# Performance work log

Hardware: AMD Instinct MI355X
Metric: run time of the kernel (lower is better)

## Reference

```python
import jax, jax.numpy as jnp
import numpy as np

N_SAMPLES = 131072
WINDOW = 2048
HOP = WINDOW // 2            # 1024
N_COEFFS = WINDOW // 2 + 1   # 1025
N_RES = 64
EXPR = 4
BASE_RES = 0.5
RES_FACTOR = 0.99
N_FRAMES = N_SAMPLES // HOP  # 128


def setup_inputs() -> dict:
    key = jax.random.key(0)
    k1, k2, k3, k4 = jax.random.split(key, 4)
    shape = (N_RES, N_COEFFS, EXPR)
    # mirrors torch init: uniform(0.01, 1) base + small deformation
    amp = jax.random.uniform(k1, shape, minval=0.01, maxval=1.0)
    phase = jax.random.uniform(k2, shape, minval=0.01, maxval=1.0)
    decay = jax.random.uniform(k3, shape, minval=0.01, maxval=1.0)
    phase_dither = jax.random.uniform(k4, shape, minval=0.01, maxval=1.0)
    return dict(amp=amp, phase=phase, decay=decay, phase_dither=phase_dither)


def _flat(x):
    # (n_res, n_coeffs, expr) -> (n_res, expr, n_coeffs) -> (n_res*expr, n_coeffs)
    return jnp.transpose(x, (0, 2, 1)).reshape(-1, N_COEFFS)


def reference(amp, phase, decay, phase_dither):
    amp_f, phase_f = _flat(amp), _flat(phase)
    decay_f, dith_f = _flat(decay), _flat(phase_dither)
    B = amp_f.shape[0]  # n_res * expr

    res_span = 1.0 - BASE_RES
    # per-bin per-frame decay coefficient in (base_resonance, ~0.995)
    coeffs = BASE_RES + jax.nn.sigmoid(decay_f) * res_span * RES_FACTOR  # (B, C)
    start_mags = amp_f ** 2                                             # (B, C)
    start_phase = jnp.tanh(phase_f) * np.pi                             # (B, C)
    dither = jnp.tanh(dith_f)                                           # (B, C)

    # frame-wise exponential decay scan: mags[t] = start_mags * coeffs**(t+1)
    t = jnp.arange(1, N_FRAMES + 1, dtype=coeffs.dtype)                 # (T,)
    mags = start_mags[:, None, :] * jnp.exp(t[None, :, None] * jnp.log(coeffs)[:, None, :])  # (B, T, C)

    # frame-wise phase accumulation with deterministic dither noise
    noise = jax.random.uniform(jax.random.key(42), (B, N_FRAMES, N_COEFFS), minval=-1.0, maxval=1.0)
    phase_step = start_phase[:, None, :] + dither[:, None, :] * noise   # (B, T, C)
    phase_acc = jnp.cumsum(phase_step, axis=1)                          # (B, T, C)

    spec = mags * jnp.exp(1j * phase_acc)                               # complex (B, T, C)
    frames = jnp.fft.irfft(spec, n=WINDOW, axis=-1)                     # (B, T, W)

    # overlap-add with hop = WINDOW // 2, no analysis window
    out = jnp.zeros((B, (N_FRAMES + 1) * HOP), dtype=frames.dtype)
    out = out.at[:, :N_FRAMES * HOP].add(frames[:, :, :HOP].reshape(B, -1))
    out = out.at[:, HOP:].add(frames[:, :, HOP:].reshape(B, -1))
    out = out[:, :N_FRAMES * HOP]                                       # (B, n_samples)

    return out.reshape(1, 1, N_RES, EXPR, N_SAMPLES)
```

## Files before the change

### kernel.cpp

```cpp
#include <hip/hip_runtime.h>
#include <math.h>

#define NRES     64
#define EXPRN    4
#define B_TOT    256
#define NC       1025
#define NF       128
#define HOP      1024
#define MHALF    1024
#define NTHREADS 512
#define CHUNK    32
#define NCHUNK   4

__device__ __forceinline__ int F(int a) { return a + (a >> 5); }

__device__ __forceinline__ uint32_t rotl32(uint32_t x, int r) {
  return (x << r) | (x >> (32 - r));
}

__device__ __forceinline__ float tf_noise(uint32_t i) {
  const uint32_t k0 = 0u, k1 = 42u;
  const uint32_t k2 = 0x1BD11BDAu ^ k0 ^ k1;
  uint32_t x0 = 0u + k0;
  uint32_t x1 = i + k1;
#define TF_ROUND(r) { x0 += x1; x1 = rotl32(x1, r); x1 ^= x0; }
  TF_ROUND(13) TF_ROUND(15) TF_ROUND(26) TF_ROUND(6)
  x0 += k1; x1 += k2 + 1u;
  TF_ROUND(17) TF_ROUND(29) TF_ROUND(16) TF_ROUND(24)
  x0 += k2; x1 += k0 + 2u;
  TF_ROUND(13) TF_ROUND(15) TF_ROUND(26) TF_ROUND(6)
  x0 += k0; x1 += k1 + 3u;
  TF_ROUND(17) TF_ROUND(29) TF_ROUND(16) TF_ROUND(24)
  x0 += k1; x1 += k2 + 4u;
  TF_ROUND(13) TF_ROUND(15) TF_ROUND(26) TF_ROUND(6)
  x0 += k2; x1 += k0 + 5u;
#undef TF_ROUND
  uint32_t bits = x0 ^ x1;
  float f = __uint_as_float((bits >> 9) | 0x3f800000u) - 1.0f;
  return f * 2.0f - 1.0f;
}

__global__ __launch_bounds__(NTHREADS, 6)
void resblock_kernel(const float* __restrict__ amp,
                     const float* __restrict__ phase,
                     const float* __restrict__ decay,
                     const float* __restrict__ pdith,
                     float* __restrict__ out) {
  __shared__ float zr[MHALF + MHALF / 32], zi[MHALF + MHALF / 32];
  __shared__ float2 tw[MHALF];

  const int tid = threadIdx.x;
  const int k = tid;
  const int b = blockIdx.x;
  const int j = blockIdx.y;
  const int t0 = j * CHUNK;
  const int tstart = (j == 0) ? 0 : (t0 - 1);
  const int tend = t0 + CHUNK;
  const int r = b >> 2, e = b & 3;
  const int base = r * (NC * EXPRN) + e;
  const float PI_F = 3.14159265358979323846f;

  for (int i = tid; i < MHALF; i += NTHREADS) {
    float cs = 1.0f, sn = 0.0f;
    if (i > 0) {
      const int half = 1 << (31 - __clz(i));
      const int rr = i - half;
      float ang = PI_F * (float)rr / (float)half;
      sincosf(ang, &sn, &cs);
    }
    tw[i] = make_float2(cs, sn);
  }

  float spA, dthA, coefA, magA, phiA; uint32_t idxA;
  float spB, dthB, coefB, magB, phiB; uint32_t idxB;
  float spM = 0, dthM = 0, coefM = 1, magM = 0, phiM = 0; uint32_t idxM = 0;

  auto load_chain = [&](int c, float& sp, float& dth, float& coef,
                        float& mag, float& phi, uint32_t& idx) {
    const int gi = base + c * EXPRN;
    const float a = amp[gi], p = phase[gi], d0 = decay[gi], pd = pdith[gi];
    const float sig = 1.0f / (1.0f + expf(-d0));
    const float coeff = 0.5f + 0.495f * sig;
    coef = coeff;
    const float lgc = logf(coeff);
    const float smN = a * a * (1.0f / 1024.0f);
    sp  = tanhf(p) * PI_F;
    dth = tanhf(pd);
    idx = (uint32_t)(b * NF) * (uint32_t)NC + (uint32_t)c;
    float acc = 0.0f;
    for (int s2 = 0; s2 < tstart; ++s2) { acc += tf_noise(idx); idx += NC; }
    phi = (float)tstart * sp + dth * acc;
    mag = smN * expf((float)tstart * lgc);
  };
  load_chain(k,         spA, dthA, coefA, magA, phiA, idxA);
  load_chain(MHALF - k, spB, dthB, coefB, magB, phiB, idxB);
  if (k == 0) load_chain(512, spM, dthM, coefM, magM, phiM, idxM);

  float stk, ctk;
  sincosf(PI_F * (float)k * (1.0f / 1024.0f), &stk, &ctk);

  float carry0 = 0.0f, carry1 = 0.0f;
  const long outbase = (long)b * (NF * HOP);
  const int krA = (int)(__brev((uint32_t)k) >> 22);
  const int krB = (int)(__brev((uint32_t)(MHALF - k)) >> 22);

  __syncthreads();

  for (int t = tstart; t < tend; ++t) {
    { float nz = tf_noise(idxA); idxA += NC; phiA += spA + dthA * nz; magA *= coefA; }
    { float nz = tf_noise(idxB); idxB += NC; phiB += spB + dthB * nz; magB *= coefB; }
    float snA, csA; __sincosf(phiA, &snA, &csA);
    float snB, csB; __sincosf(phiB, &snB, &csB);
    const float x0r = magA * csA, x0i = (k == 0) ? 0.0f : magA * snA;
    const float x1r = magB * csB, x1i = (k == 0) ? 0.0f : magB * snB;
    const float ar = 0.5f * (x0r + x1r);
    const float ai = 0.5f * (x0i - x1i);
    const float dr = x0r - x1r;
    const float di = x0i + x1i;
    const float br = -0.5f * (dr * stk + di * ctk);
    const float bi =  0.5f * (dr * ctk - di * stk);
    zr[F(krA)] = ar + br;
    zi[F(krA)] = ai + bi;
    if (k > 0) {
      zr[F(krB)] = ar - br;
      zi[F(krB)] = bi - ai;
    } else {
      float nz = tf_noise(idxM); idxM += NC; phiM += spM + dthM * nz; magM *= coefM;
      float snM, csM; __sincosf(phiM, &snM, &csM);
      zr[F(1)] =  magM * csM;
      zi[F(1)] = -magM * snM;
    }
    __syncthreads();

    for (int s = 1; s <= 10; ++s) {
      const int half = 1 << (s - 1);
      const int q  = tid >> (s - 1);
      const int rr = tid & (half - 1);
      const int i0 = (q << s) | rr;
      const int i1 = i0 + half;
      const float2 w = tw[half + rr];
      const float ur = zr[F(i0)], ui = zi[F(i0)];
      const float vr = zr[F(i1)], vi = zi[F(i1)];
      const float tr  = vr * w.x - vi * w.y;
      const float ti2 = vr * w.y + vi * w.x;
      zr[F(i0)] = ur + tr;   zi[F(i0)] = ui + ti2;
      zr[F(i1)] = ur - tr;   zi[F(i1)] = ui - ti2;
      __syncthreads();
    }

    {
      const int m0 = tid, m1 = tid + 512;
      const float xa0 = (m0 & 1) ? zi[F(m0 >> 1)] : zr[F(m0 >> 1)];
      const float xa1 = (m1 & 1) ? zi[F(m1 >> 1)] : zr[F(m1 >> 1)];
      const float xb0 = (m0 & 1) ? zi[F((m0 + HOP) >> 1)] : zr[F((m0 + HOP) >> 1)];
      const float xb1 = (m1 & 1) ? zi[F((m1 + HOP) >> 1)] : zr[F((m1 + HOP) >> 1)];
      if (t >= t0) {
        const long ob = outbase + (long)t * HOP;
        out[ob + m0] = xa0 + carry0;
        out[ob + m1] = xa1 + carry1;
      }
      carry0 = xb0;
      carry1 = xb1;
    }
    __syncthreads();
  }
}

extern "C" void kernel_launch(void* const* d_in, const int* in_sizes, int n_in,
                              void* d_out, int out_size, void* d_ws, size_t ws_size,
                              hipStream_t stream) {
  (void)in_sizes; (void)n_in; (void)d_ws; (void)ws_size; (void)out_size;
  const float* amp   = (const float*)d_in[0];
  const float* phase = (const float*)d_in[1];
  const float* decay = (const float*)d_in[2];
  const float* pdith = (const float*)d_in[3];
  float* out = (float*)d_out;

  dim3 grid(B_TOT, NCHUNK);
  dim3 block(NTHREADS);
  hipLaunchKernelGGL(resblock_kernel, grid, block, 0, stream,
                     amp, phase, decay, pdith, out);
}
```

Before: 408.1 us.

## Precompute noise prefix sums in a separate kernel and pack FFT buffer as float2

Adds a prefix kernel that computes the cumulative threefry noise sums at each chunk boundary once per (batch, bin) and stores them in the workspace. The main kernel reads those values instead of regenerating up to 95 noise samples per chain in every chunk block. The split real and imaginary shared arrays are also merged into one padded float2 array, so output pairs are read and written as float2 vectors. This adds a second launch and a workspace dependency, and changes the LDS padding pattern.

```diff
diff --git a/kernel.cpp b/kernel.cpp
--- a/kernel.cpp
+++ b/kernel.cpp
@@ -12,7 +12,7 @@
 #define CHUNK    32
 #define NCHUNK   4
 
-__device__ __forceinline__ int F(int a) { return a + (a >> 5); }
+__device__ __forceinline__ int P2(int a) { return a + (a >> 4); }
 
 __device__ __forceinline__ uint32_t rotl32(uint32_t x, int r) {
   return (x << r) | (x >> (32 - r));
@@ -40,13 +40,31 @@
   return f * 2.0f - 1.0f;
 }
 
+__global__ __launch_bounds__(256)
+void prefix_kernel(float* __restrict__ ws) {
+  const int flat = blockIdx.x * 256 + threadIdx.x;
+  const int b = flat / NC;
+  const int c = flat - b * NC;
+  uint32_t idx = (uint32_t)(b * NF) * (uint32_t)NC + (uint32_t)c;
+  float acc = 0.0f, p1 = 0.0f, p2 = 0.0f;
+  for (int s = 0; s < 95; ++s) {
+    if (s == 31) p1 = acc;
+    if (s == 63) p2 = acc;
+    acc += tf_noise(idx);
+    idx += NC;
+  }
+  float* w = ws + (size_t)flat * 3;
+  w[0] = p1; w[1] = p2; w[2] = acc;
+}
+
 __global__ __launch_bounds__(NTHREADS, 6)
 void resblock_kernel(const float* __restrict__ amp,
                      const float* __restrict__ phase,
                      const float* __restrict__ decay,
                      const float* __restrict__ pdith,
+                     const float* __restrict__ pre,
                      float* __restrict__ out) {
-  __shared__ float zr[MHALF + MHALF / 32], zi[MHALF + MHALF / 32];
+  __shared__ float2 z[MHALF + MHALF / 16];
   __shared__ float2 tw[MHALF];
 
   const int tid = threadIdx.x;
@@ -86,10 +104,9 @@
     const float smN = a * a * (1.0f / 1024.0f);
     sp  = tanhf(p) * PI_F;
     dth = tanhf(pd);
-    idx = (uint32_t)(b * NF) * (uint32_t)NC + (uint32_t)c;
-    float acc = 0.0f;
-    for (int s2 = 0; s2 < tstart; ++s2) { acc += tf_noise(idx); idx += NC; }
-    phi = (float)tstart * sp + dth * acc;
+    idx = (uint32_t)(b * NF + tstart) * (uint32_t)NC + (uint32_t)c;
+    const float P = (j == 0) ? 0.0f : pre[((size_t)b * NC + c) * 3 + (j - 1)];
+    phi = (float)tstart * sp + dth * P;
     mag = smN * expf((float)tstart * lgc);
   };
   load_chain(k,         spA, dthA, coefA, magA, phiA, idxA);
@@ -99,10 +116,10 @@
   float stk, ctk;
   sincosf(PI_F * (float)k * (1.0f / 1024.0f), &stk, &ctk);
 
-  float carry0 = 0.0f, carry1 = 0.0f;
+  float2 carry = make_float2(0.0f, 0.0f);
   const long outbase = (long)b * (NF * HOP);
-  const int krA = (int)(__brev((uint32_t)k) >> 22);
-  const int krB = (int)(__brev((uint32_t)(MHALF - k)) >> 22);
+  const int krA = P2((int)(__brev((uint32_t)k) >> 22));
+  const int krB = (k > 0) ? P2((int)(__brev((uint32_t)(MHALF - k)) >> 22)) : P2(1);
 
   __syncthreads();
 
@@ -119,16 +136,13 @@
     const float di = x0i + x1i;
     const float br = -0.5f * (dr * stk + di * ctk);
     const float bi =  0.5f * (dr * ctk - di * stk);
-    zr[F(krA)] = ar + br;
-    zi[F(krA)] = ai + bi;
+    z[krA] = make_float2(ar + br, ai + bi);
     if (k > 0) {
-      zr[F(krB)] = ar - br;
-      zi[F(krB)] = bi - ai;
+      z[krB] = make_float2(ar - br, bi - ai);
     } else {
       float nz = tf_noise(idxM); idxM += NC; phiM += spM + dthM * nz; magM *= coefM;
       float snM, csM; __sincosf(phiM, &snM, &csM);
-      zr[F(1)] =  magM * csM;
-      zi[F(1)] = -magM * snM;
+      z[krB] = make_float2(magM * csM, -magM * snM);
     }
     __syncthreads();
 
@@ -139,28 +153,23 @@
       const int i0 = (q << s) | rr;
       const int i1 = i0 + half;
       const float2 w = tw[half + rr];
-      const float ur = zr[F(i0)], ui = zi[F(i0)];
-      const float vr = zr[F(i1)], vi = zi[F(i1)];
-      const float tr  = vr * w.x - vi * w.y;
-      const float ti2 = vr * w.y + vi * w.x;
-      zr[F(i0)] = ur + tr;   zi[F(i0)] = ui + ti2;
-      zr[F(i1)] = ur - tr;   zi[F(i1)] = ui - ti2;
+      const float2 u = z[P2(i0)];
+      const float2 v = z[P2(i1)];
+      const float tr  = v.x * w.x - v.y * w.y;
+      const float ti2 = v.x * w.y + v.y * w.x;
+      z[P2(i0)] = make_float2(u.x + tr, u.y + ti2);
+      z[P2(i1)] = make_float2(u.x - tr, u.y - ti2);
       __syncthreads();
     }
 
     {
-      const int m0 = tid, m1 = tid + 512;
-      const float xa0 = (m0 & 1) ? zi[F(m0 >> 1)] : zr[F(m0 >> 1)];
-      const float xa1 = (m1 & 1) ? zi[F(m1 >> 1)] : zr[F(m1 >> 1)];
-      const float xb0 = (m0 & 1) ? zi[F((m0 + HOP) >> 1)] : zr[F((m0 + HOP) >> 1)];
-      const float xb1 = (m1 & 1) ? zi[F((m1 + HOP) >> 1)] : zr[F((m1 + HOP) >> 1)];
+      const float2 e0 = z[P2(tid)];
+      const float2 e1 = z[P2(512 + tid)];
       if (t >= t0) {
-        const long ob = outbase + (long)t * HOP;
-        out[ob + m0] = xa0 + carry0;
-        out[ob + m1] = xa1 + carry1;
+        float2* ob = (float2*)(out + outbase + (long)t * HOP) + tid;
+        *ob = make_float2(e0.x + carry.x, e0.y + carry.y);
       }
-      carry0 = xb0;
-      carry1 = xb1;
+      carry = e1;
     }
     __syncthreads();
   }
@@ -169,15 +178,18 @@
 extern "C" void kernel_launch(void* const* d_in, const int* in_sizes, int n_in,
                               void* d_out, int out_size, void* d_ws, size_t ws_size,
                               hipStream_t stream) {
-  (void)in_sizes; (void)n_in; (void)d_ws; (void)ws_size; (void)out_size;
+  (void)in_sizes; (void)n_in; (void)ws_size; (void)out_size;
   const float* amp   = (const float*)d_in[0];
   const float* phase = (const float*)d_in[1];
   const float* decay = (const float*)d_in[2];
   const float* pdith = (const float*)d_in[3];
   float* out = (float*)d_out;
+  float* pre = (float*)d_ws;
+
+  hipLaunchKernelGGL(prefix_kernel, dim3(NC), dim3(256), 0, stream, pre);
 
   dim3 grid(B_TOT, NCHUNK);
   dim3 block(NTHREADS);
   hipLaunchKernelGGL(resblock_kernel, grid, block, 0, stream,
-                     amp, phase, decay, pdith, out);
+                     amp, phase, decay, pdith, pre, out);
 }
```

Result: no change. 413.6 us (+1.4%).
